# Optimization experiments

Hardware: AMD Instinct MI355X
Metric: run time of the kernel (lower is better)

## Reference

```python
import jax, jax.numpy as jnp
import numpy as np

N = 100000   # nodes
E = 600000   # edges
F_IN = 128   # input feature dim
H = 256      # hidden_channels


def setup_inputs() -> dict:
    key = jax.random.key(0)
    ks = jax.random.split(key, 8)
    x = jax.random.normal(ks[0], (N, F_IN), dtype=jnp.float32)
    edge_index = jax.random.randint(ks[1], (2, E), 0, N, dtype=jnp.int64)
    # SAGEConv params: out = lin_l(mean_agg) + lin_r(x_root); bias only on lin_l (PyG default)
    s1 = 1.0 / np.sqrt(F_IN)
    s2 = 1.0 / np.sqrt(H)
    Wl1 = jax.random.uniform(ks[2], (F_IN, H), jnp.float32, -s1, s1)
    Wr1 = jax.random.uniform(ks[3], (F_IN, H), jnp.float32, -s1, s1)
    b1 = jnp.zeros((H,), jnp.float32)
    Wl2 = jax.random.uniform(ks[4], (H, H), jnp.float32, -s2, s2)
    Wr2 = jax.random.uniform(ks[5], (H, H), jnp.float32, -s2, s2)
    b2 = jnp.zeros((H,), jnp.float32)
    return {"x": x, "edge_index": edge_index, "Wl1": Wl1, "Wr1": Wr1, "b1": b1,
            "Wl2": Wl2, "Wr2": Wr2, "b2": b2}


def _sage_conv(h, src, dst, Wl, Wr, b):
    # mean aggregation of source-node features at destination nodes
    msg = h[src]                                             # [E, d]
    agg = jax.ops.segment_sum(msg, dst, num_segments=N)      # [N, d]
    cnt = jax.ops.segment_sum(jnp.ones((src.shape[0],), h.dtype), dst, num_segments=N)
    agg = agg / jnp.maximum(cnt, 1.0)[:, None]
    return agg @ Wl + b + h @ Wr


def reference(x, edge_index, Wl1, Wr1, b1, Wl2, Wr2, b2):
    src, dst = edge_index[0], edge_index[1]
    h = jax.nn.relu(_sage_conv(x, src, dst, Wl1, Wr1, b1))
    return _sage_conv(h, src, dst, Wl2, Wr2, b2)
```

## Files before the change

### kernel.cpp

```cpp
#include <hip/hip_runtime.h>

#define Nn 100000
#define Ee 600000
#define Fin 128
#define Hd  256
#define NB  ((Nn + 1023) / 1024)
#define CB  12500
#define PB  768
#define EB  ((Ee + 255) / 256)

typedef __attribute__((ext_vector_type(8))) short short8;
typedef __attribute__((ext_vector_type(4))) float floatx4;

__device__ __forceinline__ float bf2f(unsigned short h) {
    return __uint_as_float(((unsigned int)h) << 16);
}
__device__ __forceinline__ unsigned short f2bf(float f) {
    unsigned int u = __float_as_uint(f);
    u += 0x7FFFu + ((u >> 16) & 1u);
    return (unsigned short)(u >> 16);
}
__device__ __forceinline__ float loadf(const void* p, int i, int f32) {
    return f32 ? ((const float*)p)[i] : bf2f(((const unsigned short*)p)[i]);
}
__device__ __forceinline__ void gload_lds16(const void* g, void* lds) {
    __builtin_amdgcn_global_load_lds((const __attribute__((address_space(1))) void*)g,
                                     (__attribute__((address_space(3))) void*)lds,
                                     16, 0, 0);
}

__device__ __forceinline__ void get_edge(const int* __restrict__ ei, int is64, int e,
                                         int& s, int& d) {
    if (is64) { s = ei[2 * e]; d = ei[2 * (Ee + e)]; }
    else      { s = ei[e];     d = ei[Ee + e]; }
}

__global__ void k_init(const unsigned int* __restrict__ ei,
                       const unsigned short* __restrict__ xu,
                       int* __restrict__ flag, int* __restrict__ cnt) {
    int i = blockIdx.x * 256 + threadIdx.x;
    if (i < 2 * Nn) cnt[i] = 0;
    if (blockIdx.x == 0 && threadIdx.x == 0) {
        int is64 = 1;
        for (int k = 1; k < 64; k += 2)
            if (ei[k] != 0u) { is64 = 0; break; }
        flag[0] = is64;
        int isf32 = 0;
        for (int k = 0; k < 512; k += 2) {
            unsigned e = (xu[k] >> 7) & 0xFFu;
            if (e >= 0xC0u) { isf32 = 1; break; }
        }
        flag[1] = isf32;
    }
}

__global__ void k_pre(const void* __restrict__ x, unsigned short* __restrict__ xb,
                      const void* __restrict__ Wl1, const void* __restrict__ Wr1,
                      const void* __restrict__ Wl2, const void* __restrict__ Wr2,
                      unsigned short* __restrict__ Wt1, unsigned short* __restrict__ Wt2,
                      const int* __restrict__ ei, int* __restrict__ cnt,
                      const int* __restrict__ flag) {
    int bid = blockIdx.x;
    if (bid < CB) {
        int i = (bid * 256 + threadIdx.x) * 4;
        if (i >= Nn * Fin) return;
        if (flag[1]) {
            float4 v = ((const float4*)x)[i >> 2];
            ushort4 u;
            u.x = f2bf(v.x); u.y = f2bf(v.y); u.z = f2bf(v.z); u.w = f2bf(v.w);
            ((ushort4*)xb)[i >> 2] = u;
        } else {
            ((ushort4*)xb)[i >> 2] = ((const ushort4*)x)[i >> 2];
        }
    } else if (bid < CB + PB) {
        int f32 = flag[1];
        int tid = (bid - CB) * 256 + threadIdx.x;
        if (tid < 256 * 256) {
            int n = tid >> 8, k = tid & 255;
            float v = (k < 128) ? loadf(Wl1, k * 256 + n, f32) : loadf(Wr1, (k - 128) * 256 + n, f32);
            Wt1[n * 256 + k] = f2bf(v);
        }
        int t2 = tid - 256 * 256;
        if (t2 >= 0 && t2 < 256 * 512) {
            int n = t2 >> 9, k = t2 & 511;
            float v = (k < 256) ? loadf(Wl2, k * 256 + n, f32) : loadf(Wr2, (k - 256) * 256 + n, f32);
            Wt2[n * 512 + k] = f2bf(v);
        }
    } else {
        int e = (bid - CB - PB) * 256 + threadIdx.x;
        if (e >= Ee) return;
        int is64 = flag[0], s, d;
        get_edge(ei, is64, e, s, d);
        atomicAdd(&cnt[d], 1);
    }
}

__global__ void k_bsum(const int* __restrict__ cnt, int* __restrict__ bsum) {
    __shared__ int red[256];
    int b = blockIdx.x, t = threadIdx.x;
    int i = b * 1024 + t * 4;
    int s = 0;
    if (i + 3 < Nn) {
        int4 v = *reinterpret_cast<const int4*>(cnt + i);
        s = v.x + v.y + v.z + v.w;
    } else {
        for (int j = 0; j < 4; j++) if (i + j < Nn) s += cnt[i + j];
    }
    red[t] = s;
    __syncthreads();
    for (int off = 128; off > 0; off >>= 1) {
        if (t < off) red[t] += red[t + off];
        __syncthreads();
    }
    if (t == 0) bsum[b] = red[0];
}

__global__ void k_bscan(const int* __restrict__ bsum, int* __restrict__ bpre,
                        int* __restrict__ rowptr) {
    __shared__ int sc[128];
    int t = threadIdx.x;
    int v = (t < NB) ? bsum[t] : 0;
    sc[t] = v;
    __syncthreads();
    for (int off = 1; off < 128; off <<= 1) {
        int add = (t >= off) ? sc[t - off] : 0;
        __syncthreads();
        sc[t] += add;
        __syncthreads();
    }
    if (t < NB) bpre[t] = sc[t] - v;
    if (t == 127) rowptr[Nn] = sc[127];
}

__global__ void k_rowptr(const int* __restrict__ cnt, const int* __restrict__ bpre,
                         int* __restrict__ rowptr) {
    __shared__ int sc[256];
    int b = blockIdx.x, t = threadIdx.x;
    int i = b * 1024 + t * 4;
    int4 c = make_int4(0, 0, 0, 0);
    if (i + 3 < Nn) {
        c = *reinterpret_cast<const int4*>(cnt + i);
    } else {
        if (i     < Nn) c.x = cnt[i];
        if (i + 1 < Nn) c.y = cnt[i + 1];
        if (i + 2 < Nn) c.z = cnt[i + 2];
        if (i + 3 < Nn) c.w = cnt[i + 3];
    }
    int s = c.x + c.y + c.z + c.w;
    sc[t] = s;
    __syncthreads();
    for (int off = 1; off < 256; off <<= 1) {
        int add = (t >= off) ? sc[t - off] : 0;
        __syncthreads();
        sc[t] += add;
        __syncthreads();
    }
    int p = bpre[b] + sc[t] - s;
    int4 r;
    r.x = p;
    r.y = r.x + c.x;
    r.z = r.y + c.y;
    r.w = r.z + c.z;
    if (i + 3 < Nn) {
        *reinterpret_cast<int4*>(rowptr + i) = r;
    } else {
        if (i     < Nn) rowptr[i]     = r.x;
        if (i + 1 < Nn) rowptr[i + 1] = r.y;
        if (i + 2 < Nn) rowptr[i + 2] = r.z;
        if (i + 3 < Nn) rowptr[i + 3] = r.w;
    }
}

__global__ void k_fill(const int* __restrict__ ei, const int* __restrict__ flag,
                       const int* __restrict__ rowptr, int* __restrict__ cur,
                       int* __restrict__ srcl) {
    int e = blockIdx.x * 256 + threadIdx.x;
    if (e >= Ee) return;
    int is64 = flag[0], s, d;
    get_edge(ei, is64, e, s, d);
    int pos = atomicAdd(&cur[d], 1);
    srcl[rowptr[d] + pos] = s;
}

template <int F, int SIN, int SOUT>
__device__ __forceinline__ void agg_body(const unsigned short* __restrict__ X,
                                         unsigned short* __restrict__ O,
                                         const int* __restrict__ rowptr,
                                         const int* __restrict__ srcl) {
    int gw = (blockIdx.x * blockDim.x + threadIdx.x) >> 6;
    int lane = threadIdx.x & 63;
    if (gw >= Nn) return;
    int b = rowptr[gw], e = rowptr[gw + 1];
    constexpr int C = F / 64;
    float acc[C] = {};
    if (e > b) {
        int last = e - 1;
        for (int i = b; i < e; i += 8) {
            int sv[8];
            float w[8];
#pragma unroll
            for (int j = 0; j < 8; j++) {
                int id = i + j;
                sv[j] = srcl[id < last ? id : last];
                w[j] = (id < e) ? 1.f : 0.f;
            }
            if constexpr (C == 2) {
                ushort2 u[8];
#pragma unroll
                for (int j = 0; j < 8; j++)
                    u[j] = *reinterpret_cast<const ushort2*>(X + (size_t)sv[j] * SIN + lane * 2);
#pragma unroll
                for (int j = 0; j < 8; j++) {
                    acc[0] = fmaf(w[j], bf2f(u[j].x), acc[0]);
                    acc[1] = fmaf(w[j], bf2f(u[j].y), acc[1]);
                }
            } else {
                ushort4 u[8];
#pragma unroll
                for (int j = 0; j < 8; j++)
                    u[j] = *reinterpret_cast<const ushort4*>(X + (size_t)sv[j] * SIN + lane * 4);
#pragma unroll
                for (int j = 0; j < 8; j++) {
                    acc[0] = fmaf(w[j], bf2f(u[j].x), acc[0]);
                    acc[1] = fmaf(w[j], bf2f(u[j].y), acc[1]);
                    acc[2] = fmaf(w[j], bf2f(u[j].z), acc[2]);
                    acc[3] = fmaf(w[j], bf2f(u[j].w), acc[3]);
                }
            }
        }
    }
    float inv = 1.f / (float)max(e - b, 1);
    unsigned short* op = O + (size_t)gw * SOUT + lane * C;
    if constexpr (C == 2) {
        ushort2 u; u.x = f2bf(acc[0] * inv); u.y = f2bf(acc[1] * inv);
        *reinterpret_cast<ushort2*>(op) = u;
    } else {
        ushort4 u;
        u.x = f2bf(acc[0] * inv); u.y = f2bf(acc[1] * inv);
        u.z = f2bf(acc[2] * inv); u.w = f2bf(acc[3] * inv);
        *reinterpret_cast<ushort4*>(op) = u;
    }
}

__global__ void k_agg1(const unsigned short* __restrict__ xb, unsigned short* __restrict__ agg1,
                       const int* __restrict__ rowptr, const int* __restrict__ srcl) {
    agg_body<Fin, Fin, Fin>(xb, agg1, rowptr, srcl);
}

__global__ void k_agg2(const int* __restrict__ rowptr, const int* __restrict__ srcl,
                       unsigned short* __restrict__ acat_ws) {
    agg_body<Hd, 512, 512>(acat_ws + 256, acat_ws, rowptr, srcl);
}

template <int KT, int K1, int S1, int S2>
__device__ __forceinline__ void gemm_core_lds(const unsigned short* __restrict__ A1,
                                              const unsigned short* __restrict__ A2,
                                              const unsigned short* __restrict__ Wt,
                                              floatx4 (&acc)[4][4],
                                              unsigned short* sA, unsigned short* sB,
                                              int m_base) {
    const int tid = threadIdx.x;
    const int lane = tid & 63, wid = tid >> 6;
    const int wm = wid & 1, wn = wid >> 1;
    const int quad = lane >> 4, l16 = lane & 15;
    const int n_base = wn * 64;
    const int rs = tid >> 3;
    const int cs = tid & 7;

    for (int kb = 0; kb < KT; kb += 64) {
        __syncthreads();
#pragma unroll
        for (int i = 0; i < 2; i++) {
            int r = i * 64 + rs;
            int gk = kb + ((cs ^ (r & 7)) << 3);
            int m = m_base + r; if (m >= Nn) m = Nn - 1;
            const unsigned short* gp = (gk < K1)
                ? A1 + (size_t)m * S1 + gk
                : A2 + (size_t)m * S2 + (gk - K1);
            gload_lds16(gp, sA + i * 4096 + wid * 512);
        }
#pragma unroll
        for (int i = 0; i < 4; i++) {
            int n = i * 64 + rs;
            int gk = kb + ((cs ^ (n & 7)) << 3);
            gload_lds16(Wt + (size_t)n * KT + gk, sB + i * 4096 + wid * 512);
        }
        __syncthreads();
#pragma unroll
        for (int ks = 0; ks < 64; ks += 32) {
            short8 a[4], b[4];
            int q = (ks >> 3) + quad;
#pragma unroll
            for (int mt = 0; mt < 4; mt++) {
                int r = wm * 64 + mt * 16 + l16;
                a[mt] = *reinterpret_cast<const short8*>(
                    sA + r * 64 + ((q ^ (l16 & 7)) << 3));
            }
#pragma unroll
            for (int nt = 0; nt < 4; nt++) {
                int n = n_base + nt * 16 + l16;
                b[nt] = *reinterpret_cast<const short8*>(
                    sB + n * 64 + ((q ^ (l16 & 7)) << 3));
            }
#pragma unroll
            for (int mt = 0; mt < 4; mt++)
#pragma unroll
                for (int nt = 0; nt < 4; nt++)
                    acc[mt][nt] = __builtin_amdgcn_mfma_f32_16x16x32_bf16(a[mt], b[nt], acc[mt][nt], 0, 0, 0);
        }
    }
}

__global__ __launch_bounds__(512) void k_gemm1(const unsigned short* __restrict__ agg1,
                                               const unsigned short* __restrict__ xb,
                                               const unsigned short* __restrict__ Wt1,
                                               const void* __restrict__ bias,
                                               const int* __restrict__ flag,
                                               unsigned short* __restrict__ acat_ws) {
    __shared__ unsigned short sA[8192];
    __shared__ unsigned short sB[16384];
    int f32 = flag[1];
    int tid = threadIdx.x;
    int wid = tid >> 6, lane = tid & 63;
    int wm = wid & 1, wn = wid >> 1;
    int quad = lane >> 4, l16 = lane & 15;
    int m_base = blockIdx.x * 128;
    floatx4 acc[4][4] = {};
    gemm_core_lds<256, 128, 128, 128>(agg1, xb, Wt1, acc, sA, sB, m_base);
#pragma unroll
    for (int p = 0; p < 2; p++) {
        __syncthreads();
        if (wm == p) {
#pragma unroll
            for (int nt = 0; nt < 4; nt++) {
                int n = wn * 64 + nt * 16 + l16;
                float bv = loadf(bias, n, f32);
#pragma unroll
                for (int mt = 0; mt < 4; mt++) {
#pragma unroll
                    for (int r = 0; r < 4; r++) {
                        float v = acc[mt][nt][r] + bv;
                        v = v > 0.f ? v : 0.f;
                        sB[(mt * 16 + quad * 4 + r) * 256 + n] = f2bf(v);
                    }
                }
            }
        }
        __syncthreads();
#pragma unroll
        for (int rnd = 0; rnd < 4; rnd++) {
            int rl = rnd * 16 + (tid >> 5);
            int m = m_base + p * 64 + rl;
            if (m < Nn)
                *reinterpret_cast<short8*>(acat_ws + (size_t)m * 512 + 256 + (tid & 31) * 8) =
                    *reinterpret_cast<const short8*>(sB + rl * 256 + (tid & 31) * 8);
        }
    }
}

__global__ __launch_bounds__(512) void k_gemm2(const unsigned short* __restrict__ Wt2,
                                               const void* __restrict__ bias,
                                               const int* __restrict__ flag,
                                               const unsigned short* __restrict__ acat_ws,
                                               void* __restrict__ out) {
    __shared__ unsigned short sA[8192];
    __shared__ unsigned short sB[16384];
    int f32 = flag[1];
    int tid = threadIdx.x;
    int wid = tid >> 6, lane = tid & 63;
    int wm = wid & 1, wn = wid >> 1;
    int quad = lane >> 4, l16 = lane & 15;
    int m_base = blockIdx.x * 128;
    floatx4 acc[4][4] = {};
    gemm_core_lds<512, 512, 512, 512>(acat_ws, acat_ws, Wt2, acc, sA, sB, m_base);
    float* sF = (float*)sB;
#pragma unroll
    for (int q = 0; q < 4; q++) {
        __syncthreads();
        if (wm == (q >> 1)) {
#pragma unroll
            for (int nt = 0; nt < 4; nt++) {
                int n = wn * 64 + nt * 16 + l16;
                float bv = loadf(bias, n, f32);
#pragma unroll
                for (int mt2 = 0; mt2 < 2; mt2++) {
                    int mt = (q & 1) * 2 + mt2;
#pragma unroll
                    for (int r = 0; r < 4; r++)
                        sF[(mt2 * 16 + quad * 4 + r) * 256 + n] = acc[mt][nt][r] + bv;
                }
            }
        }
        __syncthreads();
#pragma unroll
        for (int rnd = 0; rnd < 2; rnd++) {
            int rl = rnd * 16 + (tid >> 5);
            int m = m_base + q * 32 + rl;
            if (m < Nn) {
                if (f32) {
                    float4* dst = (float4*)((float*)out + (size_t)m * 256) + (tid & 31) * 2;
                    const float4* src = (const float4*)(sF + rl * 256) + (tid & 31) * 2;
                    dst[0] = src[0];
                    dst[1] = src[1];
                } else {
                    const float* src = sF + rl * 256 + (tid & 31) * 8;
                    short8 pk;
#pragma unroll
                    for (int j = 0; j < 8; j++)
                        ((unsigned short*)&pk)[j] = f2bf(src[j]);
                    *reinterpret_cast<short8*>((unsigned short*)out + (size_t)m * 256 + (tid & 31) * 8) = pk;
                }
            }
        }
    }
}

extern "C" void kernel_launch(void* const* d_in, const int* in_sizes, int n_in,
                              void* d_out, int out_size, void* d_ws, size_t ws_size,
                              hipStream_t stream) {
    const void* x   = d_in[0];
    const int*  ei  = (const int*)d_in[1];
    const void* Wl1 = d_in[2];
    const void* Wr1 = d_in[3];
    const void* b1  = d_in[4];
    const void* Wl2 = d_in[5];
    const void* Wr2 = d_in[6];
    const void* b2  = d_in[7];

    char* ws = (char*)d_ws;
    size_t off_cnt    = 0;
    size_t off_cur    = off_cnt + (size_t)Nn * 4;
    size_t off_rowptr = off_cur + (size_t)Nn * 4;
    size_t off_srcl   = off_rowptr + (size_t)(Nn + 4) * 4;
    size_t off_flag   = off_srcl + (size_t)Ee * 4;
    size_t off_bsum   = ((off_flag + 8 + 255) / 256) * 256;
    size_t off_bpre   = off_bsum + 128 * 4;
    size_t off_wt1    = off_bpre + 128 * 4;
    size_t off_wt2    = off_wt1 + 256 * 256 * 2;
    size_t off_xb     = off_wt2 + 256 * 512 * 2;
    size_t off_agg1   = off_xb + (size_t)Nn * Fin * 2;
    size_t off_acat   = off_agg1 + (size_t)Nn * Fin * 2;

    int*            cnt     = (int*)(ws + off_cnt);
    int*            cur     = (int*)(ws + off_cur);
    int*            rowptr  = (int*)(ws + off_rowptr);
    int*            srcl    = (int*)(ws + off_srcl);
    int*            flag    = (int*)(ws + off_flag);
    int*            bsum    = (int*)(ws + off_bsum);
    int*            bpre    = (int*)(ws + off_bpre);
    unsigned short* Wt1     = (unsigned short*)(ws + off_wt1);
    unsigned short* Wt2     = (unsigned short*)(ws + off_wt2);
    unsigned short* xb      = (unsigned short*)(ws + off_xb);
    unsigned short* agg1    = (unsigned short*)(ws + off_agg1);
    unsigned short* acat_ws = (unsigned short*)(ws + off_acat);

    k_init<<<(2 * Nn + 255) / 256, 256, 0, stream>>>((const unsigned int*)ei,
                                                     (const unsigned short*)x, flag, cnt);
    k_pre<<<CB + PB + EB, 256, 0, stream>>>(x, xb, Wl1, Wr1, Wl2, Wr2, Wt1, Wt2,
                                            ei, cnt, flag);
    k_bsum<<<NB, 256, 0, stream>>>(cnt, bsum);
    k_bscan<<<1, 128, 0, stream>>>(bsum, bpre, rowptr);
    k_rowptr<<<NB, 256, 0, stream>>>(cnt, bpre, rowptr);
    k_fill<<<EB, 256, 0, stream>>>(ei, flag, rowptr, cur, srcl);

    int ab = (Nn * 64 + 255) / 256;
    int gx = (Nn + 127) / 128;

    k_agg1<<<ab, 256, 0, stream>>>(xb, agg1, rowptr, srcl);
    k_gemm1<<<gx, 512, 0, stream>>>(agg1, xb, Wt1, b1, flag, acat_ws);
    k_agg2<<<ab, 256, 0, stream>>>(rowptr, srcl, acat_ws);
    k_gemm2<<<gx, 512, 0, stream>>>(Wt2, b2, flag, acat_ws, d_out);
}
```

Baseline: 379.9 us.

## Split GEMM output columns across two 256-thread blocks and parallelize flag detection

Both GEMM kernels now use 256-thread blocks that each compute a 128x128 output tile, with two blocks per 128-row strip covering the two column halves. Grid size doubles and LDS per block shrinks, which should raise occupancy and the number of blocks in flight. The cost is that each A tile is loaded twice, once per column half. The init kernel's serial single-thread format detection is replaced with a wave-wide ballot over sampled inputs.

New measurement: 387.1 us. Within noise of the previous version (+1.9%).

```diff
diff --git a/kernel.cpp b/kernel.cpp
--- a/kernel.cpp
+++ b/kernel.cpp
@@ -40,17 +40,18 @@
                        int* __restrict__ flag, int* __restrict__ cnt) {
     int i = blockIdx.x * 256 + threadIdx.x;
     if (i < 2 * Nn) cnt[i] = 0;
-    if (blockIdx.x == 0 && threadIdx.x == 0) {
-        int is64 = 1;
-        for (int k = 1; k < 64; k += 2)
-            if (ei[k] != 0u) { is64 = 0; break; }
-        flag[0] = is64;
-        int isf32 = 0;
-        for (int k = 0; k < 512; k += 2) {
-            unsigned e = (xu[k] >> 7) & 0xFFu;
-            if (e >= 0xC0u) { isf32 = 1; break; }
-        }
-        flag[1] = isf32;
+    if (blockIdx.x == 0 && threadIdx.x < 64) {
+        int l = threadIdx.x;
+        unsigned hi = (l < 32) ? ei[2 * l + 1] : 0u;
+        unsigned long long nz = __ballot(hi != 0u);
+        int big = 0;
+#pragma unroll
+        for (int j = 0; j < 4; j++) {
+            unsigned u = xu[l * 8 + j * 2];
+            if (((u >> 7) & 0xFFu) >= 0xC0u) big = 1;
+        }
+        unsigned long long bb = __ballot(big != 0);
+        if (l == 0) { flag[0] = (nz == 0ull) ? 1 : 0; flag[1] = (bb != 0ull) ? 1 : 0; }
     }
 }
 
@@ -263,27 +264,26 @@
     const int lane = tid & 63, wid = tid >> 6;
     const int wm = wid & 1, wn = wid >> 1;
     const int quad = lane >> 4, l16 = lane & 15;
-    const int n_base = wn * 64;
-    const int rs = tid >> 3;
-    const int cs = tid & 7;
+    const int rs2 = lane >> 3;
+    const int cs = lane & 7;
 
     for (int kb = 0; kb < KT; kb += 64) {
         __syncthreads();
 #pragma unroll
-        for (int i = 0; i < 2; i++) {
-            int r = i * 64 + rs;
+        for (int i = 0; i < 4; i++) {
+            int r = i * 32 + wid * 8 + rs2;
             int gk = kb + ((cs ^ (r & 7)) << 3);
             int m = m_base + r; if (m >= Nn) m = Nn - 1;
             const unsigned short* gp = (gk < K1)
                 ? A1 + (size_t)m * S1 + gk
                 : A2 + (size_t)m * S2 + (gk - K1);
-            gload_lds16(gp, sA + i * 4096 + wid * 512);
+            gload_lds16(gp, sA + i * 2048 + wid * 512);
         }
 #pragma unroll
         for (int i = 0; i < 4; i++) {
-            int n = i * 64 + rs;
+            int n = i * 32 + wid * 8 + rs2;
             int gk = kb + ((cs ^ (n & 7)) << 3);
-            gload_lds16(Wt + (size_t)n * KT + gk, sB + i * 4096 + wid * 512);
+            gload_lds16(Wt + (size_t)n * KT + gk, sB + i * 2048 + wid * 512);
         }
         __syncthreads();
 #pragma unroll
@@ -298,7 +298,7 @@
             }
 #pragma unroll
             for (int nt = 0; nt < 4; nt++) {
-                int n = n_base + nt * 16 + l16;
+                int n = wn * 64 + nt * 16 + l16;
                 b[nt] = *reinterpret_cast<const short8*>(
                     sB + n * 64 + ((q ^ (l16 & 7)) << 3));
             }
@@ -311,22 +311,24 @@
     }
 }
 
-__global__ __launch_bounds__(512) void k_gemm1(const unsigned short* __restrict__ agg1,
+__global__ __launch_bounds__(256) void k_gemm1(const unsigned short* __restrict__ agg1,
                                                const unsigned short* __restrict__ xb,
                                                const unsigned short* __restrict__ Wt1,
                                                const void* __restrict__ bias,
                                                const int* __restrict__ flag,
                                                unsigned short* __restrict__ acat_ws) {
     __shared__ unsigned short sA[8192];
-    __shared__ unsigned short sB[16384];
+    __shared__ unsigned short sB[8192];
     int f32 = flag[1];
     int tid = threadIdx.x;
     int wid = tid >> 6, lane = tid & 63;
     int wm = wid & 1, wn = wid >> 1;
     int quad = lane >> 4, l16 = lane & 15;
-    int m_base = blockIdx.x * 128;
+    int mb = blockIdx.x >> 1, nb = blockIdx.x & 1;
+    int m_base = mb * 128;
     floatx4 acc[4][4] = {};
-    gemm_core_lds<256, 128, 128, 128>(agg1, xb, Wt1, acc, sA, sB, m_base);
+    gemm_core_lds<256, 128, 128, 128>(agg1, xb, Wt1 + (size_t)nb * 128 * 256,
+                                      acc, sA, sB, m_base);
 #pragma unroll
     for (int p = 0; p < 2; p++) {
         __syncthreads();
@@ -334,14 +336,14 @@
 #pragma unroll
             for (int nt = 0; nt < 4; nt++) {
                 int n = wn * 64 + nt * 16 + l16;
-                float bv = loadf(bias, n, f32);
+                float bv = loadf(bias, nb * 128 + n, f32);
 #pragma unroll
                 for (int mt = 0; mt < 4; mt++) {
 #pragma unroll
                     for (int r = 0; r < 4; r++) {
                         float v = acc[mt][nt][r] + bv;
                         v = v > 0.f ? v : 0.f;
-                        sB[(mt * 16 + quad * 4 + r) * 256 + n] = f2bf(v);
+                        sB[(mt * 16 + quad * 4 + r) * 128 + n] = f2bf(v);
                     }
                 }
             }
@@ -349,66 +351,65 @@
         __syncthreads();
 #pragma unroll
         for (int rnd = 0; rnd < 4; rnd++) {
-            int rl = rnd * 16 + (tid >> 5);
+            int rl = rnd * 16 + (tid >> 4);
             int m = m_base + p * 64 + rl;
             if (m < Nn)
-                *reinterpret_cast<short8*>(acat_ws + (size_t)m * 512 + 256 + (tid & 31) * 8) =
-                    *reinterpret_cast<const short8*>(sB + rl * 256 + (tid & 31) * 8);
-        }
-    }
-}
-
-__global__ __launch_bounds__(512) void k_gemm2(const unsigned short* __restrict__ Wt2,
+                *reinterpret_cast<short8*>(acat_ws + (size_t)m * 512 + 256 + nb * 128 + (tid & 15) * 8) =
+                    *reinterpret_cast<const short8*>(sB + rl * 128 + (tid & 15) * 8);
+        }
+    }
+}
+
+__global__ __launch_bounds__(256) void k_gemm2(const unsigned short* __restrict__ Wt2,
                                                const void* __restrict__ bias,
                                                const int* __restrict__ flag,
                                                const unsigned short* __restrict__ acat_ws,
                                                void* __restrict__ out) {
-    __shared__ unsigned short sA[8192];
-    __shared__ unsigned short sB[16384];
+    __shared__ unsigned short sMem[16384];
+    unsigned short* sA = sMem;
+    unsigned short* sB = sMem + 8192;
     int f32 = flag[1];
     int tid = threadIdx.x;
     int wid = tid >> 6, lane = tid & 63;
     int wm = wid & 1, wn = wid >> 1;
     int quad = lane >> 4, l16 = lane & 15;
-    int m_base = blockIdx.x * 128;
+    int mb = blockIdx.x >> 1, nb = blockIdx.x & 1;
+    int m_base = mb * 128;
     floatx4 acc[4][4] = {};
-    gemm_core_lds<512, 512, 512, 512>(acat_ws, acat_ws, Wt2, acc, sA, sB, m_base);
-    float* sF = (float*)sB;
-#pragma unroll
-    for (int q = 0; q < 4; q++) {
-        __syncthreads();
-        if (wm == (q >> 1)) {
+    gemm_core_lds<512, 512, 512, 512>(acat_ws, acat_ws, Wt2 + (size_t)nb * 128 * 512,
+                                      acc, sA, sB, m_base);
+    float* sF = (float*)sMem;
+#pragma unroll
+    for (int p = 0; p < 2; p++) {
+        __syncthreads();
+        if (wm == p) {
 #pragma unroll
             for (int nt = 0; nt < 4; nt++) {
                 int n = wn * 64 + nt * 16 + l16;
-                float bv = loadf(bias, n, f32);
-#pragma unroll
-                for (int mt2 = 0; mt2 < 2; mt2++) {
-                    int mt = (q & 1) * 2 + mt2;
+                float bv = loadf(bias, nb * 128 + n, f32);
+#pragma unroll
+                for (int mt = 0; mt < 4; mt++) {
 #pragma unroll
                     for (int r = 0; r < 4; r++)
-                        sF[(mt2 * 16 + quad * 4 + r) * 256 + n] = acc[mt][nt][r] + bv;
+                        sF[(mt * 16 + quad * 4 + r) * 128 + n] = acc[mt][nt][r] + bv;
                 }
             }
         }
         __syncthreads();
 #pragma unroll
-        for (int rnd = 0; rnd < 2; rnd++) {
-            int rl = rnd * 16 + (tid >> 5);
-            int m = m_base + q * 32 + rl;
+        for (int rnd = 0; rnd < 8; rnd++) {
+            int rl = rnd * 8 + (tid >> 5);
+            int m = m_base + p * 64 + rl;
             if (m < Nn) {
                 if (f32) {
-                    float4* dst = (float4*)((float*)out + (size_t)m * 256) + (tid & 31) * 2;
-                    const float4* src = (const float4*)(sF + rl * 256) + (tid & 31) * 2;
-                    dst[0] = src[0];
-                    dst[1] = src[1];
+                    *((float4*)((float*)out + (size_t)m * 256 + nb * 128) + (tid & 31)) =
+                        *((const float4*)(sF + rl * 128) + (tid & 31));
                 } else {
-                    const float* src = sF + rl * 256 + (tid & 31) * 8;
-                    short8 pk;
-#pragma unroll
-                    for (int j = 0; j < 8; j++)
-                        ((unsigned short*)&pk)[j] = f2bf(src[j]);
-                    *reinterpret_cast<short8*>((unsigned short*)out + (size_t)m * 256 + (tid & 31) * 8) = pk;
+                    const float* src = sF + rl * 128 + (tid & 31) * 4;
+                    ushort4 pk;
+                    pk.x = f2bf(src[0]); pk.y = f2bf(src[1]);
+                    pk.z = f2bf(src[2]); pk.w = f2bf(src[3]);
+                    *reinterpret_cast<ushort4*>((unsigned short*)out + (size_t)m * 256 + nb * 128 + (tid & 31) * 4) = pk;
                 }
             }
         }
@@ -464,10 +465,10 @@
     k_fill<<<EB, 256, 0, stream>>>(ei, flag, rowptr, cur, srcl);
 
     int ab = (Nn * 64 + 255) / 256;
-    int gx = (Nn + 127) / 128;
+    int gx = ((Nn + 127) / 128) * 2;
 
     k_agg1<<<ab, 256, 0, stream>>>(xb, agg1, rowptr, srcl);
-    k_gemm1<<<gx, 512, 0, stream>>>(agg1, xb, Wt1, b1, flag, acat_ws);
+    k_gemm1<<<gx, 256, 0, stream>>>(agg1, xb, Wt1, b1, flag, acat_ws);
     k_agg2<<<ab, 256, 0, stream>>>(rowptr, srcl, acat_ws);
-    k_gemm2<<<gx, 512, 0, stream>>>(Wt2, b2, flag, acat_ws, d_out);
-}
+    k_gemm2<<<gx, 256, 0, stream>>>(Wt2, b2, flag, acat_ws, d_out);
+}
```
